# Kernel tuning notes

Hardware: AMD Instinct MI355X
Metric: run time of the kernel (lower is better)

## Reference

```python
import jax, jax.numpy as jnp
import numpy as np

VOCAB, EMBED, HIDDEN, NCLS = 50257, 512, 1024, 5


def setup_inputs() -> dict:
    key = jax.random.key(0)
    ks = jax.random.split(key, 8)
    s_e = 1.0 / np.sqrt(EMBED)
    s_h = 1.0 / np.sqrt(HIDDEN)
    emb = jax.random.normal(ks[0], (VOCAB, EMBED), jnp.float32)
    emb = emb.at[0].set(0.0)  # padding_idx=0
    return {
        "x": jax.random.randint(ks[1], (64, 512), 0, VOCAB, jnp.int32),
        "emb_table": emb,
        "W_ih": jax.random.uniform(ks[2], (4 * HIDDEN, EMBED), jnp.float32, -s_h, s_h),
        "W_hh": jax.random.uniform(ks[3], (4 * HIDDEN, HIDDEN), jnp.float32, -s_h, s_h),
        "b_ih": jax.random.uniform(ks[4], (4 * HIDDEN,), jnp.float32, -s_h, s_h),
        "b_hh": jax.random.uniform(ks[5], (4 * HIDDEN,), jnp.float32, -s_h, s_h),
        "W_fc": jax.random.uniform(ks[6], (NCLS, HIDDEN), jnp.float32, -s_h, s_h),
        "b_fc": jax.random.uniform(ks[7], (NCLS,), jnp.float32, -s_h, s_h),
    }


def _lstm(xe, W_ih, W_hh, b_ih, b_hh):
    # xe: [B,T,E] -> outputs [B,T,H]; PyTorch gate order i,f,g,o
    B, T, _ = xe.shape
    H = W_hh.shape[1]
    x_gates = jnp.einsum('bte,ge->btg', xe, W_ih) + (b_ih + b_hh)  # [B,T,4H]
    x_gates = jnp.transpose(x_gates, (1, 0, 2))  # [T,B,4H]

    def step(carry, xg):
        h, c = carry
        g = xg + h @ W_hh.T
        i, f, gg, o = jnp.split(g, 4, axis=-1)
        c = jax.nn.sigmoid(f) * c + jax.nn.sigmoid(i) * jnp.tanh(gg)
        h = jax.nn.sigmoid(o) * jnp.tanh(c)
        return (h, c), h

    init = (jnp.zeros((B, H), xe.dtype), jnp.zeros((B, H), xe.dtype))
    _, hs = jax.lax.scan(step, init, x_gates)  # hs: [T,B,H]
    return jnp.transpose(hs, (1, 0, 2))


def reference(x, emb_table, W_ih, W_hh, b_ih, b_hh, W_fc, b_fc):
    emb = emb_table.at[0].set(0.0)  # enforce padding row zero
    xe = emb[x]  # [B,T,E]
    out = _lstm(xe, W_ih, W_hh, b_ih, b_hh)  # [B,T,H]
    feat = jnp.max(out, axis=1)  # [B,H]
    return feat @ W_fc.T + b_fc  # [B,NCLS]
```

## Files before the change

kernel.cpp:

```cpp
#include <hip/hip_runtime.h>

#define BB 64
#define TT 512
#define EE 512
#define HH 1024
#define NCLS 5
#define NWG 128

typedef __attribute__((ext_vector_type(8))) short bfrag;
typedef __attribute__((ext_vector_type(4))) float facc;

#define XE_OFF   0
#define HBUF_OFF (XE_OFF + (size_t)TT * BB * EE * 2)
#define FEAT_OFF (HBUF_OFF + (size_t)2 * BB * HH * 2)
#define SYNC_OFF (FEAT_OFF + (size_t)BB * HH * 4)

static __device__ __forceinline__ unsigned short f2bf(float f) {
  unsigned int u = __float_as_uint(f);
  u += 0x7fff + ((u >> 16) & 1);
  return (unsigned short)(u >> 16);
}

static __device__ __forceinline__ void st_u32_sys(unsigned int* p, unsigned int v) {
  asm volatile("global_store_dword %0, %1, off sc0 sc1" :: "v"(p), "v"(v) : "memory");
}
static __device__ __forceinline__ unsigned int ld_u32_sys(const unsigned int* p) {
  unsigned int r;
  asm volatile("global_load_dword %0, %1, off sc0 sc1\n\t"
               "s_waitcnt vmcnt(0)" : "=v"(r) : "v"(p) : "memory");
  return r;
}

__global__ __launch_bounds__(256) void k_gather(const int* __restrict__ x,
                                                const float* __restrict__ emb,
                                                unsigned short* __restrict__ xe,
                                                int* __restrict__ sync) {
  if (blockIdx.x == 0 && threadIdx.x < 256) sync[threadIdx.x] = 0;
  int wave = (blockIdx.x * 256 + threadIdx.x) >> 6;
  int lane = threadIdx.x & 63;
  int t = wave >> 6;
  int b = wave & 63;
  int tok = x[b * TT + t];
  const float* src = emb + (size_t)tok * EE + lane * 8;
  float4 f0 = ((const float4*)src)[0];
  float4 f1 = ((const float4*)src)[1];
  uint4 pk;
  pk.x = (unsigned)f2bf(f0.x) | ((unsigned)f2bf(f0.y) << 16);
  pk.y = (unsigned)f2bf(f0.z) | ((unsigned)f2bf(f0.w) << 16);
  pk.z = (unsigned)f2bf(f1.x) | ((unsigned)f2bf(f1.y) << 16);
  pk.w = (unsigned)f2bf(f1.z) | ((unsigned)f2bf(f1.w) << 16);
  *(uint4*)(xe + ((size_t)t * BB + b) * EE + lane * 8) = pk;
}

__global__ __launch_bounds__(256, 1) void k_lstm(const float* __restrict__ W_ih,
                                                 const float* __restrict__ W_hh,
                                                 const float* __restrict__ b_ih,
                                                 const float* __restrict__ b_hh,
                                                 const unsigned short* __restrict__ xe,
                                                 unsigned short* __restrict__ hbuf,
                                                 float* __restrict__ feat,
                                                 int* __restrict__ sync) {
  __shared__ unsigned short Wlds[32][1544];
  __shared__ float bias_lds[32];

  const int w = blockIdx.x;
  const int tid = threadIdx.x;

  for (int idx = tid; idx < 32 * 512; idx += 256) {
    int r = idx >> 9, k = idx & 511;
    int R = (r >> 3) * 1024 + w * 8 + (r & 7);
    Wlds[r][k] = f2bf(W_ih[(size_t)R * EE + k]);
  }
  for (int idx = tid; idx < 32 * 1024; idx += 256) {
    int r = idx >> 10, k = idx & 1023;
    int R = (r >> 3) * 1024 + w * 8 + (r & 7);
    Wlds[r][512 + k] = f2bf(W_hh[(size_t)R * HH + k]);
  }
  if (tid < 32) {
    int R = (tid >> 3) * 1024 + w * 8 + (tid & 7);
    bias_lds[tid] = b_ih[R] + b_hh[R];
  }
  __syncthreads();

  const int lane = tid & 63;
  const int wm = tid >> 6;
  const int c15 = lane & 15;
  const int kq = lane >> 4;
  const int k0 = kq * 8;
  const int bA = wm * 16 + c15;

  const unsigned short* wl0 = &Wlds[c15][k0];
  const unsigned short* wl1 = &Wlds[16 + c15][k0];
  const float bias0 = bias_lds[c15];
  const float bias1 = bias_lds[16 + c15];

  float cst[4]  = {0.f, 0.f, 0.f, 0.f};
  float hmax[4] = {-1e30f, -1e30f, -1e30f, -1e30f};

  unsigned short* h0 = hbuf;
  unsigned short* h1 = hbuf + BB * HH;
  unsigned int* flags = (unsigned int*)sync;
  unsigned int* gen   = (unsigned int*)(sync + 200);

  const size_t xe_lane = (size_t)bA * EE + k0;
  const size_t h_lane  = (size_t)bA * HH + k0;

  for (int t = 0; t < TT; ++t) {
    facc a0 = {0.f,0.f,0.f,0.f}, a1 = a0, a2 = a0, a3 = a0;
    const unsigned short* xet = xe + (size_t)t * (BB * EE) + xe_lane;

#pragma unroll 4
    for (int kk = 0; kk < 16; kk += 2) {
      bfrag A  = *(const bfrag*)(xet + kk * 32);
      bfrag B0 = *(const bfrag*)(wl0 + kk * 32);
      bfrag B1 = *(const bfrag*)(wl1 + kk * 32);
      a0 = __builtin_amdgcn_mfma_f32_16x16x32_bf16(A, B0, a0, 0, 0, 0);
      a2 = __builtin_amdgcn_mfma_f32_16x16x32_bf16(A, B1, a2, 0, 0, 0);
      bfrag A2  = *(const bfrag*)(xet + kk * 32 + 32);
      bfrag B0b = *(const bfrag*)(wl0 + kk * 32 + 32);
      bfrag B1b = *(const bfrag*)(wl1 + kk * 32 + 32);
      a1 = __builtin_amdgcn_mfma_f32_16x16x32_bf16(A2, B0b, a1, 0, 0, 0);
      a3 = __builtin_amdgcn_mfma_f32_16x16x32_bf16(A2, B1b, a3, 0, 0, 0);
    }

    if (t > 0) {
      if (w == 0 && tid < NWG) {
        const unsigned int* fp = flags + tid;
        while (ld_u32_sys(fp) < (unsigned)t) {}
      }
      __syncthreads();
      if (w == 0 && tid == 0) st_u32_sys(gen, (unsigned)t);
      if (tid == 0) {
        while (ld_u32_sys(gen) < (unsigned)t) {}
      }
      __syncthreads();

      const unsigned short* hp = ((t & 1) ? h1 : h0) + h_lane;
      bfrag hA[32];
#pragma unroll
      for (int i = 0; i < 32; ++i)
        asm volatile("global_load_dwordx4 %0, %1, off sc0 sc1"
                     : "=v"(hA[i]) : "v"(hp + i * 32));
      __builtin_amdgcn_sched_barrier(0);
      asm volatile("s_waitcnt vmcnt(0)" ::: "memory");
      __builtin_amdgcn_sched_barrier(0);

#pragma unroll
      for (int kk = 0; kk < 32; kk += 2) {
        bfrag B0 = *(const bfrag*)(wl0 + 512 + kk * 32);
        bfrag B1 = *(const bfrag*)(wl1 + 512 + kk * 32);
        a0 = __builtin_amdgcn_mfma_f32_16x16x32_bf16(hA[kk], B0, a0, 0, 0, 0);
        a2 = __builtin_amdgcn_mfma_f32_16x16x32_bf16(hA[kk], B1, a2, 0, 0, 0);
        bfrag B0b = *(const bfrag*)(wl0 + 512 + (kk + 1) * 32);
        bfrag B1b = *(const bfrag*)(wl1 + 512 + (kk + 1) * 32);
        a1 = __builtin_amdgcn_mfma_f32_16x16x32_bf16(hA[kk + 1], B0b, a1, 0, 0, 0);
        a3 = __builtin_amdgcn_mfma_f32_16x16x32_bf16(hA[kk + 1], B1b, a3, 0, 0, 0);
      }
    }

    facc X = a0 + a1;
    facc Y = a2 + a3;
    unsigned int hb[4];
#pragma unroll
    for (int j = 0; j < 4; ++j) {
      float xv = X[j] + bias0;
      float yv = Y[j] + bias1;
      float xs = __shfl_xor(xv, 8, 64);
      float ys = __shfl_xor(yv, 8, 64);
      bool lo = (c15 < 8);
      float vi = lo ? xv : xs;
      float vf = lo ? xs : xv;
      float vg = lo ? yv : ys;
      float vo = lo ? ys : yv;
      float sf = 1.f / (1.f + __expf(-vf));
      float si = 1.f / (1.f + __expf(-vi));
      float eg = __expf(-2.f * fabsf(vg));
      float tg = copysignf((1.f - eg) / (1.f + eg), vg);
      float cc = sf * cst[j] + si * tg;
      cst[j] = cc;
      float so = 1.f / (1.f + __expf(-vo));
      float ec = __expf(-2.f * fabsf(cc));
      float tc = copysignf((1.f - ec) / (1.f + ec), cc);
      float hh = so * tc;
      hmax[j] = fmaxf(hmax[j], hh);
      hb[j] = f2bf(hh);
    }

    if (t < TT - 1) {
      unsigned int* hn32 = (unsigned int*)(((t & 1) ? h0 : h1));
#pragma unroll
      for (int j = 0; j < 4; ++j) {
        unsigned int part = (unsigned int)__shfl_xor((int)hb[j], 1, 64);
        if ((c15 & 1) == 0 && c15 < 8) {
          unsigned int v = (hb[j] & 0xffffu) | (part << 16);
          unsigned int* p = hn32 + (size_t)(wm * 16 + kq * 4 + j) * (HH / 2)
                                 + w * 4 + (c15 >> 1);
          st_u32_sys(p, v);
        }
      }
      asm volatile("s_waitcnt vmcnt(0)" ::: "memory");
      __syncthreads();
      if (tid == 0) st_u32_sys(flags + w, (unsigned)(t + 1));
    }
  }

  if (c15 < 8) {
    int jh = w * 8 + c15;
#pragma unroll
    for (int j = 0; j < 4; ++j)
      feat[(size_t)(wm * 16 + kq * 4 + j) * HH + jh] = hmax[j];
  }
}

__global__ __launch_bounds__(64) void k_fc(const float* __restrict__ feat,
                                           const float* __restrict__ W_fc,
                                           const float* __restrict__ b_fc,
                                           float* __restrict__ out) {
  int b = blockIdx.x, cls = blockIdx.y;
  int lane = threadIdx.x;
  const float* f  = feat + (size_t)b * HH;
  const float* wr = W_fc + (size_t)cls * HH;
  float s = 0.f;
  for (int k = lane; k < HH; k += 64) s = fmaf(f[k], wr[k], s);
#pragma unroll
  for (int off = 32; off > 0; off >>= 1) s += __shfl_down(s, off, 64);
  if (lane == 0) out[b * NCLS + cls] = s + b_fc[cls];
}

extern "C" void kernel_launch(void* const* d_in, const int* in_sizes, int n_in,
                              void* d_out, int out_size, void* d_ws, size_t ws_size,
                              hipStream_t stream) {
  const int*   x    = (const int*)d_in[0];
  const float* emb  = (const float*)d_in[1];
  const float* W_ih = (const float*)d_in[2];
  const float* W_hh = (const float*)d_in[3];
  const float* b_ih = (const float*)d_in[4];
  const float* b_hh = (const float*)d_in[5];
  const float* W_fc = (const float*)d_in[6];
  const float* b_fc = (const float*)d_in[7];
  float* out = (float*)d_out;

  char* ws = (char*)d_ws;
  unsigned short* xe   = (unsigned short*)(ws + XE_OFF);
  unsigned short* hbuf = (unsigned short*)(ws + HBUF_OFF);
  float*          feat = (float*)(ws + FEAT_OFF);
  int*            sync = (int*)(ws + SYNC_OFF);

  k_gather<<<dim3(8192), dim3(256), 0, stream>>>(x, emb, xe, sync);
  k_lstm<<<dim3(NWG), dim3(256), 0, stream>>>(W_ih, W_hh, b_ih, b_hh, xe, hbuf, feat, sync);
  k_fc<<<dim3(BB, NCLS), dim3(64), 0, stream>>>(feat, W_fc, b_fc, out);
}
```

Measured before the change: 4.893 ms.

## Replace two-level grid barrier with per-wave flag polling and per-timestep h buffers

Drops the centralized barrier, where workgroup 0 polled all flags and then published a generation counter. Instead every wave polls all 128 producer flags directly with two loads per lane and __any. When the workspace is large enough, each timestep's h is written to its own buffer, so plain cached loads can be used instead of system-coherent ones without stale reuse. This removes one sync hop per step, at the cost of a much larger hbuf footprint and heavier flag polling traffic.

```diff
diff --git a/kernel.cpp b/kernel.cpp
--- a/kernel.cpp
+++ b/kernel.cpp
@@ -10,10 +10,11 @@
 typedef __attribute__((ext_vector_type(8))) short bfrag;
 typedef __attribute__((ext_vector_type(4))) float facc;
 
-#define XE_OFF   0
-#define HBUF_OFF (XE_OFF + (size_t)TT * BB * EE * 2)
-#define FEAT_OFF (HBUF_OFF + (size_t)2 * BB * HH * 2)
-#define SYNC_OFF (FEAT_OFF + (size_t)BB * HH * 4)
+#define XE_BYTES   ((size_t)TT * BB * EE * 2)
+#define FEAT_BYTES ((size_t)BB * HH * 4)
+#define SYNC_BYTES ((size_t)4096)
+#define HBUF_FULL  ((size_t)TT * BB * HH * 2)
+#define HBUF_SMALL ((size_t)2 * BB * HH * 2)
 
 static __device__ __forceinline__ unsigned short f2bf(float f) {
   unsigned int u = __float_as_uint(f);
@@ -29,6 +30,14 @@
   asm volatile("global_load_dword %0, %1, off sc0 sc1\n\t"
                "s_waitcnt vmcnt(0)" : "=v"(r) : "v"(p) : "memory");
   return r;
+}
+static __device__ __forceinline__ void ld2_u32_sys(const unsigned int* p0,
+                                                   const unsigned int* p1,
+                                                   unsigned int& a, unsigned int& b) {
+  asm volatile("global_load_dword %0, %2, off sc0 sc1\n\t"
+               "global_load_dword %1, %3, off sc0 sc1\n\t"
+               "s_waitcnt vmcnt(0)"
+               : "=v"(a), "=v"(b) : "v"(p0), "v"(p1) : "memory");
 }
 
 __global__ __launch_bounds__(256) void k_gather(const int* __restrict__ x,
@@ -52,6 +61,7 @@
   *(uint4*)(xe + ((size_t)t * BB + b) * EE + lane * 8) = pk;
 }
 
+template <bool FULLT>
 __global__ __launch_bounds__(256, 1) void k_lstm(const float* __restrict__ W_ih,
                                                  const float* __restrict__ W_hh,
                                                  const float* __restrict__ b_ih,
@@ -97,13 +107,12 @@
   float cst[4]  = {0.f, 0.f, 0.f, 0.f};
   float hmax[4] = {-1e30f, -1e30f, -1e30f, -1e30f};
 
-  unsigned short* h0 = hbuf;
-  unsigned short* h1 = hbuf + BB * HH;
   unsigned int* flags = (unsigned int*)sync;
-  unsigned int* gen   = (unsigned int*)(sync + 200);
 
   const size_t xe_lane = (size_t)bA * EE + k0;
   const size_t h_lane  = (size_t)bA * HH + k0;
+  const unsigned int* fp0 = flags + lane;
+  const unsigned int* fp1 = flags + 64 + lane;
 
   for (int t = 0; t < TT; ++t) {
     facc a0 = {0.f,0.f,0.f,0.f}, a1 = a0, a2 = a0, a3 = a0;
@@ -124,37 +133,48 @@
     }
 
     if (t > 0) {
-      if (w == 0 && tid < NWG) {
-        const unsigned int* fp = flags + tid;
-        while (ld_u32_sys(fp) < (unsigned)t) {}
-      }
-      __syncthreads();
-      if (w == 0 && tid == 0) st_u32_sys(gen, (unsigned)t);
-      if (tid == 0) {
-        while (ld_u32_sys(gen) < (unsigned)t) {}
-      }
-      __syncthreads();
-
-      const unsigned short* hp = ((t & 1) ? h1 : h0) + h_lane;
-      bfrag hA[32];
-#pragma unroll
-      for (int i = 0; i < 32; ++i)
-        asm volatile("global_load_dwordx4 %0, %1, off sc0 sc1"
-                     : "=v"(hA[i]) : "v"(hp + i * 32));
+      unsigned int fa, fb;
+      do {
+        ld2_u32_sys(fp0, fp1, fa, fb);
+      } while (__any((int)(min(fa, fb) < (unsigned)t)));
       __builtin_amdgcn_sched_barrier(0);
-      asm volatile("s_waitcnt vmcnt(0)" ::: "memory");
-      __builtin_amdgcn_sched_barrier(0);
-
-#pragma unroll
-      for (int kk = 0; kk < 32; kk += 2) {
-        bfrag B0 = *(const bfrag*)(wl0 + 512 + kk * 32);
-        bfrag B1 = *(const bfrag*)(wl1 + 512 + kk * 32);
-        a0 = __builtin_amdgcn_mfma_f32_16x16x32_bf16(hA[kk], B0, a0, 0, 0, 0);
-        a2 = __builtin_amdgcn_mfma_f32_16x16x32_bf16(hA[kk], B1, a2, 0, 0, 0);
-        bfrag B0b = *(const bfrag*)(wl0 + 512 + (kk + 1) * 32);
-        bfrag B1b = *(const bfrag*)(wl1 + 512 + (kk + 1) * 32);
-        a1 = __builtin_amdgcn_mfma_f32_16x16x32_bf16(hA[kk + 1], B0b, a1, 0, 0, 0);
-        a3 = __builtin_amdgcn_mfma_f32_16x16x32_bf16(hA[kk + 1], B1b, a3, 0, 0, 0);
+
+      if constexpr (FULLT) {
+        const unsigned short* hp = hbuf + (size_t)t * (BB * HH) + h_lane;
+#pragma unroll 4
+        for (int kk = 0; kk < 32; kk += 2) {
+          bfrag A  = *(const bfrag*)(hp + kk * 32);
+          bfrag B0 = *(const bfrag*)(wl0 + 512 + kk * 32);
+          bfrag B1 = *(const bfrag*)(wl1 + 512 + kk * 32);
+          a0 = __builtin_amdgcn_mfma_f32_16x16x32_bf16(A, B0, a0, 0, 0, 0);
+          a2 = __builtin_amdgcn_mfma_f32_16x16x32_bf16(A, B1, a2, 0, 0, 0);
+          bfrag A2  = *(const bfrag*)(hp + kk * 32 + 32);
+          bfrag B0b = *(const bfrag*)(wl0 + 512 + (kk + 1) * 32);
+          bfrag B1b = *(const bfrag*)(wl1 + 512 + (kk + 1) * 32);
+          a1 = __builtin_amdgcn_mfma_f32_16x16x32_bf16(A2, B0b, a1, 0, 0, 0);
+          a3 = __builtin_amdgcn_mfma_f32_16x16x32_bf16(A2, B1b, a3, 0, 0, 0);
+        }
+      } else {
+        const unsigned short* hp = hbuf + ((t & 1) ? (size_t)(BB * HH) : 0) + h_lane;
+        bfrag hA[32];
+#pragma unroll
+        for (int i = 0; i < 32; ++i)
+          asm volatile("global_load_dwordx4 %0, %1, off sc0 sc1"
+                       : "=v"(hA[i]) : "v"(hp + i * 32));
+        __builtin_amdgcn_sched_barrier(0);
+        asm volatile("s_waitcnt vmcnt(0)" ::: "memory");
+        __builtin_amdgcn_sched_barrier(0);
+#pragma unroll
+        for (int kk = 0; kk < 32; kk += 2) {
+          bfrag B0 = *(const bfrag*)(wl0 + 512 + kk * 32);
+          bfrag B1 = *(const bfrag*)(wl1 + 512 + kk * 32);
+          a0 = __builtin_amdgcn_mfma_f32_16x16x32_bf16(hA[kk], B0, a0, 0, 0, 0);
+          a2 = __builtin_amdgcn_mfma_f32_16x16x32_bf16(hA[kk], B1, a2, 0, 0, 0);
+          bfrag B0b = *(const bfrag*)(wl0 + 512 + (kk + 1) * 32);
+          bfrag B1b = *(const bfrag*)(wl1 + 512 + (kk + 1) * 32);
+          a1 = __builtin_amdgcn_mfma_f32_16x16x32_bf16(hA[kk + 1], B0b, a1, 0, 0, 0);
+          a3 = __builtin_amdgcn_mfma_f32_16x16x32_bf16(hA[kk + 1], B1b, a3, 0, 0, 0);
+        }
       }
     }
 
@@ -187,7 +207,11 @@
     }
 
     if (t < TT - 1) {
-      unsigned int* hn32 = (unsigned int*)(((t & 1) ? h0 : h1));
+      unsigned int* hn32;
+      if constexpr (FULLT)
+        hn32 = (unsigned int*)(hbuf + (size_t)(t + 1) * (BB * HH));
+      else
+        hn32 = (unsigned int*)(hbuf + ((t & 1) ? 0 : (size_t)(BB * HH)));
 #pragma unroll
       for (int j = 0; j < 4; ++j) {
         unsigned int part = (unsigned int)__shfl_xor((int)hb[j], 1, 64);
@@ -241,12 +265,17 @@
   float* out = (float*)d_out;
 
   char* ws = (char*)d_ws;
-  unsigned short* xe   = (unsigned short*)(ws + XE_OFF);
-  unsigned short* hbuf = (unsigned short*)(ws + HBUF_OFF);
-  float*          feat = (float*)(ws + FEAT_OFF);
-  int*            sync = (int*)(ws + SYNC_OFF);
+  unsigned short* xe   = (unsigned short*)(ws);
+  float*          feat = (float*)(ws + XE_BYTES);
+  int*            sync = (int*)(ws + XE_BYTES + FEAT_BYTES);
+  unsigned short* hbuf = (unsigned short*)(ws + XE_BYTES + FEAT_BYTES + SYNC_BYTES);
+
+  const bool full = (ws_size >= XE_BYTES + FEAT_BYTES + SYNC_BYTES + HBUF_FULL);
 
   k_gather<<<dim3(8192), dim3(256), 0, stream>>>(x, emb, xe, sync);
-  k_lstm<<<dim3(NWG), dim3(256), 0, stream>>>(W_ih, W_hh, b_ih, b_hh, xe, hbuf, feat, sync);
+  if (full)
+    k_lstm<true><<<dim3(NWG), dim3(256), 0, stream>>>(W_ih, W_hh, b_ih, b_hh, xe, hbuf, feat, sync);
+  else
+    k_lstm<false><<<dim3(NWG), dim3(256), 0, stream>>>(W_ih, W_hh, b_ih, b_hh, xe, hbuf, feat, sync);
   k_fc<<<dim3(BB, NCLS), dim3(64), 0, stream>>>(feat, W_fc, b_fc, out);
 }
```

Measured after the change: 4.847 ms. Within noise of the previous version (-1.0%).
